# Kernel tuning notes

Measured on AMD Instinct MI355X. Metric: run time of the kernel, lower is better.

## Reference

```python
import jax, jax.numpy as jnp
import numpy as np

NUM_CAPSULE = 16
DIM_CAPSULE = 16
NUM_ROUTING = 3
EPS = 1e-7  # K.epsilon()


def squash(v, axis=-1):
    s2 = jnp.sum(jnp.square(v), axis=axis, keepdims=True) + EPS
    scale = s2 / ((1.0 + s2) * jnp.sqrt(s2))
    return scale * v


def setup_inputs() -> dict:
    key = jax.random.key(0)
    k1, k2 = jax.random.split(key)
    B, N, IC, ID = 64, 128, 32, 8
    x = jax.random.normal(k1, (B, N, IC, ID), dtype=jnp.float32)
    # glorot_uniform for W: [IC, ID, NUM_CAPSULE*DIM_CAPSULE]
    fan_in, fan_out = ID, NUM_CAPSULE * DIM_CAPSULE
    limit = np.sqrt(6.0 / (fan_in + fan_out))
    W = jax.random.uniform(k2, (IC, ID, NUM_CAPSULE * DIM_CAPSULE), dtype=jnp.float32,
                           minval=-limit, maxval=limit)
    return {"x": x, "W": W}


def reference(x, W):
    B, N, IC, ID = x.shape
    NC, DC = NUM_CAPSULE, DIM_CAPSULE
    u = x.reshape(-1, IC, ID)  # [BN, IC, ID]
    # prediction vectors: [BN, IC, NC*DC] -> [BN, NC, IC, DC]
    u_hat = jnp.einsum('bij,ijk->bik', u, W).reshape(-1, IC, NC, DC).transpose(0, 2, 1, 3)
    u_hat_stopped = jax.lax.stop_gradient(u_hat)
    b = jnp.zeros((u_hat.shape[0], NC, IC), dtype=x.dtype)
    outputs = None
    for i in range(NUM_ROUTING):
        c = jax.nn.softmax(b, axis=1)  # softmax over num_capsule axis (dim=1 in source)
        hat = u_hat if i == NUM_ROUTING - 1 else u_hat_stopped
        outputs = squash(jnp.einsum('bci,bcid->bcd', c, hat))  # [BN, NC, DC]
        if i < NUM_ROUTING - 1:
            b = b + jnp.einsum('bcd,bcid->bci', outputs, u_hat_stopped)
    return outputs.reshape(B, N, NC, DC)
```

## Files before the change

### kernel.cpp

```cpp
#include <hip/hip_runtime.h>
#include <hip/hip_bf16.h>


#define S 2

typedef float    v2f __attribute__((ext_vector_type(2)));
typedef _Float16 v2h __attribute__((ext_vector_type(2)));

template <int CTRL>
__device__ __forceinline__ float dppf(float x) {
  return __builtin_bit_cast(float,
      __builtin_amdgcn_update_dpp(0, __builtin_bit_cast(int, x), CTRL, 0xF, 0xF, true));
}
template <int CTRL>
__device__ __forceinline__ v2f dpp2(v2f v) {
  v2f r;
  r.x = dppf<CTRL>(v.x);
  r.y = dppf<CTRL>(v.y);
  return r;
}
__device__ __forceinline__ float swz4(float x) {
  return __builtin_bit_cast(float,
      __builtin_amdgcn_ds_swizzle(__builtin_bit_cast(int, x), 0x101F));
}
__device__ __forceinline__ v2f swz4_2(v2f v) {
  v2f r;
  r.x = swz4(v.x);
  r.y = swz4(v.y);
  return r;
}

#if __has_builtin(__builtin_amdgcn_fdot2)
__device__ __forceinline__ float dot2(v2h a, v2h b, float c) {
  return __builtin_amdgcn_fdot2(a, b, c, false);
}
#else
__device__ __forceinline__ float dot2(v2h a, v2h b, float c) {
  return fmaf((float)a.x, (float)b.x, fmaf((float)a.y, (float)b.y, c));
}
#endif

__global__ __launch_bounds__(256) void wt_kernel(const float* __restrict__ W,
                                                 _Float16* __restrict__ Wth) {
  int o  = blockIdx.x * 256 + threadIdx.x;
  int ic = o >> 11;
  int k  = (o >> 3) & 255;
  int id = o & 7;
  Wth[o] = (_Float16)W[(ic * 8 + id) * 256 + k];
}

__global__ __launch_bounds__(256) void xh_kernel(const float* __restrict__ x,
                                                 _Float16* __restrict__ xh) {
  int tid = blockIdx.x * 256 + threadIdx.x;
  const float4* xp = (const float4*)x + tid * 2;
  float4 f0 = xp[0], f1 = xp[1];
  v2h h0 = {(_Float16)f0.x, (_Float16)f0.y};
  v2h h1 = {(_Float16)f0.z, (_Float16)f0.w};
  v2h h2 = {(_Float16)f1.x, (_Float16)f1.y};
  v2h h3 = {(_Float16)f1.z, (_Float16)f1.w};
  uint4 o;
  o.x = __builtin_bit_cast(unsigned, h0);
  o.y = __builtin_bit_cast(unsigned, h1);
  o.z = __builtin_bit_cast(unsigned, h2);
  o.w = __builtin_bit_cast(unsigned, h3);
  ((uint4*)xh)[tid] = o;
}

__device__ __forceinline__ v2f squash2(v2f o) {
  v2f s2 = o * o;
  s2 += dpp2<0xB1>(s2);
  s2 += dpp2<0x4E>(s2);
  s2 += dpp2<0x141>(s2);
  s2 += dpp2<0x140>(s2);
  s2 += (v2f){1e-7f, 1e-7f};
  v2f sc;
  sc.x = s2.x * __builtin_amdgcn_rsqf(s2.x) * __builtin_amdgcn_rcpf(1.f + s2.x);
  sc.y = s2.y * __builtin_amdgcn_rsqf(s2.y) * __builtin_amdgcn_rcpf(1.f + s2.y);
  return o * sc;
}

template <bool ASSIGN>
__device__ __forceinline__ void b_update2(v2f v, const v2f* uh2, int dc,
                                          float* bp0, float* bp1) {
#pragma unroll
  for (int icb = 0; icb < 32; icb += 16) {
    v2f a[16];
#pragma unroll
    for (int j = 0; j < 16; ++j) a[j] = v * uh2[icb + j];
    v2f b8[8];
    const bool u8 = (dc & 8) != 0;
#pragma unroll
    for (int j = 0; j < 8; ++j) {
      v2f send = u8 ? a[j] : a[j + 8];
      v2f recv = dpp2<0x128>(send);
      b8[j] = (u8 ? a[j + 8] : a[j]) + recv;
    }
    v2f c4[4];
    const bool u4 = (dc & 4) != 0;
#pragma unroll
    for (int j = 0; j < 4; ++j) {
      v2f send = u4 ? b8[j] : b8[j + 4];
      v2f recv = swz4_2(send);
      c4[j] = (u4 ? b8[j + 4] : b8[j]) + recv;
    }
    v2f d2[2];
    const bool u2 = (dc & 2) != 0;
#pragma unroll
    for (int j = 0; j < 2; ++j) {
      v2f send = u2 ? c4[j] : c4[j + 2];
      v2f recv = dpp2<0x4E>(send);
      d2[j] = (u2 ? c4[j + 2] : c4[j]) + recv;
    }
    const bool u1 = (dc & 1) != 0;
    v2f send = u1 ? d2[0] : d2[1];
    v2f recv = dpp2<0xB1>(send);
    v2f e = (u1 ? d2[1] : d2[0]) + recv;
    if (ASSIGN) { bp0[icb + dc] = e.x;  bp1[icb + dc] = e.y; }
    else        { bp0[icb + dc] += e.x; bp1[icb + dc] += e.y; }
  }
}

__global__ __launch_bounds__(256, 3) void caps_kernel(const _Float16* __restrict__ xh,
                                                      const uint4* __restrict__ Wt4,
                                                      float* __restrict__ out) {
  const int t  = threadIdx.x;
  const int nc = t >> 4;
  const int dc = t & 15;
  const int s0 = blockIdx.x * S;

  __shared__ float b_lds[S][16][33];
  __shared__ __align__(16) float c_lds[16][68];

  v2f uh2[32];
  v2f o2 = (v2f){0.f, 0.f};

  const v2h* xp0 = (const v2h*)(xh + (s0 + 0) * 256);
  const v2h* xp1 = (const v2h*)(xh + (s0 + 1) * 256);
#pragma unroll
  for (int ic = 0; ic < 32; ++ic) {
    uint4 wv = Wt4[ic * 256 + t];
    v2h w0 = __builtin_bit_cast(v2h, wv.x);
    v2h w1 = __builtin_bit_cast(v2h, wv.y);
    v2h w2 = __builtin_bit_cast(v2h, wv.z);
    v2h w3 = __builtin_bit_cast(v2h, wv.w);
    float a0 = dot2(xp0[ic * 4 + 3], w3,
               dot2(xp0[ic * 4 + 2], w2,
               dot2(xp0[ic * 4 + 1], w1,
               dot2(xp0[ic * 4 + 0], w0, 0.f))));
    float a1 = dot2(xp1[ic * 4 + 3], w3,
               dot2(xp1[ic * 4 + 2], w2,
               dot2(xp1[ic * 4 + 1], w1,
               dot2(xp1[ic * 4 + 0], w0, 0.f))));
    v2f u = (v2f){a0, a1};
    uh2[ic] = u;
    o2 += u;
  }

  {
    v2f v = squash2(o2 * (v2f){0.0625f, 0.0625f});
    b_update2<true>(v, uh2, dc, &b_lds[0][nc][0], &b_lds[1][nc][0]);
  }
  __syncthreads();

#pragma unroll
  for (int r = 1; r < 3; ++r) {
    {
      const int ss  = t >> 7;
      const int icc = (t >> 2) & 31;
      const int q   = t & 3;
      float e0 = __expf(b_lds[ss][4 * q + 0][icc]);
      float e1 = __expf(b_lds[ss][4 * q + 1][icc]);
      float e2 = __expf(b_lds[ss][4 * q + 2][icc]);
      float e3 = __expf(b_lds[ss][4 * q + 3][icc]);
      float ps = (e0 + e1) + (e2 + e3);
      ps += dppf<0xB1>(ps);
      ps += dppf<0x4E>(ps);
      float inv = __builtin_amdgcn_rcpf(ps);
      c_lds[4 * q + 0][2 * icc + ss] = e0 * inv;
      c_lds[4 * q + 1][2 * icc + ss] = e1 * inv;
      c_lds[4 * q + 2][2 * icc + ss] = e2 * inv;
      c_lds[4 * q + 3][2 * icc + ss] = e3 * inv;
    }
    __syncthreads();

    const float4* cp = (const float4*)&c_lds[nc][0];
    v2f o = (v2f){0.f, 0.f};
#pragma unroll
    for (int j = 0; j < 16; ++j) {
      float4 cc = cp[j];
      o = __builtin_elementwise_fma((v2f){cc.x, cc.y}, uh2[2 * j + 0], o);
      o = __builtin_elementwise_fma((v2f){cc.z, cc.w}, uh2[2 * j + 1], o);
    }
    v2f v = squash2(o);
    if (r == 2) {
      out[(s0 + 0) * 256 + t] = v.x;
      out[(s0 + 1) * 256 + t] = v.y;
    } else {
      b_update2<false>(v, uh2, dc, &b_lds[0][nc][0], &b_lds[1][nc][0]);
    }
    __syncthreads();
  }
}

extern "C" void kernel_launch(void* const* d_in, const int* in_sizes, int n_in,
                              void* d_out, int out_size, void* d_ws, size_t ws_size,
                              hipStream_t stream) {
  const float* x = (const float*)d_in[0];
  const float* W = (const float*)d_in[1];
  _Float16* Wth = (_Float16*)d_ws;
  _Float16* xh  = (_Float16*)d_ws + 65536;

  wt_kernel<<<256, 256, 0, stream>>>(W, Wth);
  xh_kernel<<<1024, 256, 0, stream>>>(x, xh);
  caps_kernel<<<8192 / S, 256, 0, stream>>>(xh, (const uint4*)Wth, (float*)d_out);
}
```

Measured before the change: 98.95 us.

## XOR-permute input-capsule order per lane to simplify transpose-reduction in b update

```diff
diff --git a/kernel.cpp b/kernel.cpp
--- a/kernel.cpp
+++ b/kernel.cpp
@@ -42,11 +42,12 @@
 
 __global__ __launch_bounds__(256) void wt_kernel(const float* __restrict__ W,
                                                  _Float16* __restrict__ Wth) {
-  int o  = blockIdx.x * 256 + threadIdx.x;
-  int ic = o >> 11;
-  int k  = (o >> 3) & 255;
-  int id = o & 7;
-  Wth[o] = (_Float16)W[(ic * 8 + id) * 256 + k];
+  int o       = blockIdx.x * 256 + threadIdx.x;
+  int ic_slot = o >> 11;
+  int k       = (o >> 3) & 255;
+  int id      = o & 7;
+  int ic_src  = (ic_slot & 16) | ((ic_slot ^ k) & 15);
+  Wth[o] = (_Float16)W[(ic_src * 8 + id) * 256 + k];
 }
 
 __global__ __launch_bounds__(256) void xh_kernel(const float* __restrict__ x,
@@ -80,43 +81,22 @@
 }
 
 template <bool ASSIGN>
-__device__ __forceinline__ void b_update2(v2f v, const v2f* uh2, int dc,
+__device__ __forceinline__ void b_update2(v2f v, const v2f* uhx, int dc,
                                           float* bp0, float* bp1) {
 #pragma unroll
   for (int icb = 0; icb < 32; icb += 16) {
-    v2f a[16];
+    v2f y[16];
 #pragma unroll
-    for (int j = 0; j < 16; ++j) a[j] = v * uh2[icb + j];
-    v2f b8[8];
-    const bool u8 = (dc & 8) != 0;
+    for (int j = 0; j < 16; ++j) y[j] = v * uhx[icb + j];
 #pragma unroll
-    for (int j = 0; j < 8; ++j) {
-      v2f send = u8 ? a[j] : a[j + 8];
-      v2f recv = dpp2<0x128>(send);
-      b8[j] = (u8 ? a[j + 8] : a[j]) + recv;
-    }
-    v2f c4[4];
-    const bool u4 = (dc & 4) != 0;
+    for (int j = 0; j < 8; ++j) y[j] += dpp2<0x128>(y[j + 8]);
 #pragma unroll
-    for (int j = 0; j < 4; ++j) {
-      v2f send = u4 ? b8[j] : b8[j + 4];
-      v2f recv = swz4_2(send);
-      c4[j] = (u4 ? b8[j + 4] : b8[j]) + recv;
-    }
-    v2f d2[2];
-    const bool u2 = (dc & 2) != 0;
+    for (int j = 0; j < 4; ++j) y[j] += swz4_2(y[j + 4]);
 #pragma unroll
-    for (int j = 0; j < 2; ++j) {
-      v2f send = u2 ? c4[j] : c4[j + 2];
-      v2f recv = dpp2<0x4E>(send);
-      d2[j] = (u2 ? c4[j + 2] : c4[j]) + recv;
-    }
-    const bool u1 = (dc & 1) != 0;
-    v2f send = u1 ? d2[0] : d2[1];
-    v2f recv = dpp2<0xB1>(send);
-    v2f e = (u1 ? d2[1] : d2[0]) + recv;
-    if (ASSIGN) { bp0[icb + dc] = e.x;  bp1[icb + dc] = e.y; }
-    else        { bp0[icb + dc] += e.x; bp1[icb + dc] += e.y; }
+    for (int j = 0; j < 2; ++j) y[j] += dpp2<0x4E>(y[j + 2]);
+    y[0] += dpp2<0xB1>(y[1]);
+    if (ASSIGN) { bp0[icb + dc] = y[0].x;  bp1[icb + dc] = y[0].y; }
+    else        { bp0[icb + dc] += y[0].x; bp1[icb + dc] += y[0].y; }
   }
 }
 
@@ -129,9 +109,9 @@
   const int s0 = blockIdx.x * S;
 
   __shared__ float b_lds[S][16][33];
-  __shared__ __align__(16) float c_lds[16][68];
+  __shared__ float c_lds[16][66];
 
-  v2f uh2[32];
+  v2f uhx[32];
   v2f o2 = (v2f){0.f, 0.f};
 
   const v2h* xp0 = (const v2h*)(xh + (s0 + 0) * 256);
@@ -143,22 +123,23 @@
     v2h w1 = __builtin_bit_cast(v2h, wv.y);
     v2h w2 = __builtin_bit_cast(v2h, wv.z);
     v2h w3 = __builtin_bit_cast(v2h, wv.w);
-    float a0 = dot2(xp0[ic * 4 + 3], w3,
-               dot2(xp0[ic * 4 + 2], w2,
-               dot2(xp0[ic * 4 + 1], w1,
-               dot2(xp0[ic * 4 + 0], w0, 0.f))));
-    float a1 = dot2(xp1[ic * 4 + 3], w3,
-               dot2(xp1[ic * 4 + 2], w2,
-               dot2(xp1[ic * 4 + 1], w1,
-               dot2(xp1[ic * 4 + 0], w0, 0.f))));
+    const int icx0 = (ic & 16) | ((ic ^ dc) & 15);
+    float a0 = dot2(xp0[icx0 * 4 + 3], w3,
+               dot2(xp0[icx0 * 4 + 2], w2,
+               dot2(xp0[icx0 * 4 + 1], w1,
+               dot2(xp0[icx0 * 4 + 0], w0, 0.f))));
+    float a1 = dot2(xp1[icx0 * 4 + 3], w3,
+               dot2(xp1[icx0 * 4 + 2], w2,
+               dot2(xp1[icx0 * 4 + 1], w1,
+               dot2(xp1[icx0 * 4 + 0], w0, 0.f))));
     v2f u = (v2f){a0, a1};
-    uh2[ic] = u;
+    uhx[ic] = u;
     o2 += u;
   }
 
   {
     v2f v = squash2(o2 * (v2f){0.0625f, 0.0625f});
-    b_update2<true>(v, uh2, dc, &b_lds[0][nc][0], &b_lds[1][nc][0]);
+    b_update2<true>(v, uhx, dc, &b_lds[0][nc][0], &b_lds[1][nc][0]);
   }
   __syncthreads();
 
@@ -183,22 +164,24 @@
     }
     __syncthreads();
 
-    const float4* cp = (const float4*)&c_lds[nc][0];
+    const float2* cpair = (const float2*)&c_lds[nc][0];
     v2f o = (v2f){0.f, 0.f};
 #pragma unroll
     for (int j = 0; j < 16; ++j) {
-      float4 cc = cp[j];
-      o = __builtin_elementwise_fma((v2f){cc.x, cc.y}, uh2[2 * j + 0], o);
-      o = __builtin_elementwise_fma((v2f){cc.z, cc.w}, uh2[2 * j + 1], o);
+      const int m = j ^ dc;
+      float2 cA = cpair[m];
+      float2 cB = cpair[m + 16];
+      o = __builtin_elementwise_fma((v2f){cA.x, cA.y}, uhx[j], o);
+      o = __builtin_elementwise_fma((v2f){cB.x, cB.y}, uhx[16 + j], o);
     }
     v2f v = squash2(o);
     if (r == 2) {
       out[(s0 + 0) * 256 + t] = v.x;
       out[(s0 + 1) * 256 + t] = v.y;
     } else {
-      b_update2<false>(v, uh2, dc, &b_lds[0][nc][0], &b_lds[1][nc][0]);
+      b_update2<false>(v, uhx, dc, &b_lds[0][nc][0], &b_lds[1][nc][0]);
+      __syncthreads();
     }
-    __syncthreads();
   }
 }
 
```

New measurement: 111.8 us. 1.13x slower.
